# Optimization experiments

Hardware: AMD Instinct MI355X
Metric: run time of the kernel (lower is better)

The kernel has to match this reference:

```python
import jax, jax.numpy as jnp
import numpy as np

N, E, IN_DIM, H, C = 100000, 1600000, 128, 4, 64
NEG_SLOPE = 0.2
BN_EPS = 1e-5


def setup_inputs() -> dict:
    key = jax.random.key(0)
    ks = jax.random.split(key, 9)
    s = 1.0 / np.sqrt(IN_DIM)
    return {
        "feature": jax.random.normal(ks[0], (N, IN_DIM), dtype=jnp.float32),
        "edge_index": jax.random.randint(ks[1], (2, E), 0, N, dtype=jnp.int64),
        "W_l": jax.random.uniform(ks[2], (IN_DIM, H * C), jnp.float32, -s, s),
        "b_l": jnp.zeros((H * C,), jnp.float32),
        "W_r": jax.random.uniform(ks[3], (IN_DIM, H * C), jnp.float32, -s, s),
        "b_r": jnp.zeros((H * C,), jnp.float32),
        "att": jax.random.normal(ks[4], (H, C), dtype=jnp.float32) * 0.1,
        "bias": jnp.zeros((H * C,), jnp.float32),
        "gamma": jnp.ones((H * C,), jnp.float32),
        "beta": jnp.zeros((H * C,), jnp.float32),
    }


def reference(feature, edge_index, W_l, b_l, W_r, b_r, att, bias, gamma, beta):
    n = feature.shape[0]
    # add self loops (add_self_loops=True)
    loops = jnp.arange(n, dtype=edge_index.dtype)
    src = jnp.concatenate([edge_index[0], loops])
    dst = jnp.concatenate([edge_index[1], loops])
    # GATv2: separate source/target linear projections -> [N, H, C]
    x_l = (feature @ W_l + b_l).reshape(n, H, C)
    x_r = (feature @ W_r + b_r).reshape(n, H, C)
    # per-edge attention score: a^T LeakyReLU(x_l[src] + x_r[dst])  [Etot, H]
    e = jax.nn.leaky_relu(x_l[src] + x_r[dst], NEG_SLOPE)
    alpha = jnp.einsum('ehc,hc->eh', e, att)
    # segment softmax over incoming edges per target node
    amax = jax.ops.segment_max(alpha, dst, num_segments=n)  # [N, H]
    alpha = jnp.exp(alpha - amax[dst])
    denom = jax.ops.segment_sum(alpha, dst, num_segments=n)  # [N, H]
    alpha = alpha / (denom[dst] + 1e-16)
    # weighted scatter-aggregate of source messages
    out = jax.ops.segment_sum(x_l[src] * alpha[:, :, None], dst, num_segments=n)
    out = out.reshape(n, H * C) + bias  # concat=True
    # BatchNorm1d (training: batch statistics over nodes)
    mean = out.mean(axis=0)
    var = out.var(axis=0)
    out = (out - mean) / jnp.sqrt(var + BN_EPS) * gamma + beta
    return jax.nn.relu(out)
```

## Files before the change

### kernel.cpp

```cpp
#include <hip/hip_runtime.h>
#include <cstdint>

#define IN_DIM 128
#define HC 256
#define NEG_SLOPE 0.2f
#define BN_EPS 1e-5f
#define LOG2E 1.44269504088896340736f

#define B_HIST 1536
#define B_CW 32
#define B_FILL 512
#define CNT_STRIDE 16

typedef short bf16x8 __attribute__((ext_vector_type(8)));
typedef float f32x4 __attribute__((ext_vector_type(4)));

#define EXP2F(x) __builtin_amdgcn_exp2f(x)

__device__ __forceinline__ unsigned short f2bf(float f) {
    union { float f; unsigned int u; } v; v.f = f;
    unsigned int r = (v.u + 0x7FFFu + ((v.u >> 16) & 1u)) >> 16;
    return (unsigned short)r;
}
__device__ __forceinline__ float bf2f(unsigned short h) {
    union { unsigned int u; float f; } v; v.u = ((unsigned int)h) << 16;
    return v.f;
}

template<int CTRL>
__device__ __forceinline__ float dppadd(float x) {
    int y = __builtin_amdgcn_update_dpp(0, __builtin_bit_cast(int, x), CTRL, 0xF, 0xF, true);
    return x + __builtin_bit_cast(float, y);
}
__device__ __forceinline__ float red16(float p) {
    p = dppadd<0xB1>(p);
    p = dppadd<0x4E>(p);
    p = dppadd<0x124>(p);
    p = dppadd<0x128>(p);
    return p;
}

__device__ __forceinline__ void unpk(ushort4 u, float* f) {
    f[0] = bf2f(u.x); f[1] = bf2f(u.y); f[2] = bf2f(u.z); f[3] = bf2f(u.w);
}
__device__ __forceinline__ float esc(const float* f, float x0, float x1, float x2, float x3,
                                     float4 a) {
    float z0 = f[0] + x0, z1 = f[1] + x1, z2 = f[2] + x2, z3 = f[3] + x3;
    float p = a.x * fmaxf(z0, NEG_SLOPE * z0);
    p = fmaf(a.y, fmaxf(z1, NEG_SLOPE * z1), p);
    p = fmaf(a.z, fmaxf(z2, NEG_SLOPE * z2), p);
    p = fmaf(a.w, fmaxf(z3, NEG_SLOPE * z3), p);
    return p;
}

__global__ __launch_bounds__(256) void phase1(
    const float* __restrict__ F, unsigned short* __restrict__ Afrag,
    const float* __restrict__ Wl, const float* __restrict__ Wr,
    unsigned short* __restrict__ Wfrag,
    const int* __restrict__ ei, int* __restrict__ cnt, int* __restrict__ rank,
    int E, int n, int ntiles)
{
    int b = blockIdx.x;
    if (b < B_HIST) {
        for (int e = b * 256 + threadIdx.x; e < E; e += B_HIST * 256) {
            int dst = ei[(size_t)E + e];
            rank[e] = atomicAdd(&cnt[dst * CNT_STRIDE], 1);
        }
    } else if (b < B_HIST + B_CW) {
        int ob = (b - B_HIST) * 4 + (threadIdx.x >> 6);
        int j = ob >> 2;
        int kk = ob & 3;
        int l = threadIdx.x & 63;
        int col = j * 16 + (l & 15);
        const float* W = (col < 256) ? Wl : Wr;
        int c = col & 255;
        unsigned short tmp[8];
#pragma unroll
        for (int m = 0; m < 8; ++m) {
            int k = kk * 32 + ((l >> 4) << 3) + m;
            tmp[m] = f2bf(W[(size_t)k * 256 + c]);
        }
        ulonglong2* dst = (ulonglong2*)(Wfrag + ((size_t)(j * 4 + kk) * 64 + l) * 8);
        *dst = *(ulonglong2*)tmp;
    } else {
        int i = b - B_HIST - B_CW;
        int kk = threadIdx.x >> 6;
        int l = threadIdx.x & 63;
        int row = i * 16 + (l & 15);
        int k0 = kk * 32 + ((l >> 4) << 3);
        float4 f0 = make_float4(0.f, 0.f, 0.f, 0.f), f1 = f0;
        if (row < n) {
            const float* p = F + (size_t)row * IN_DIM + k0;
            f0 = *(const float4*)p;
            f1 = *(const float4*)(p + 4);
        }
        unsigned short tmp[8];
        tmp[0] = f2bf(f0.x); tmp[1] = f2bf(f0.y); tmp[2] = f2bf(f0.z); tmp[3] = f2bf(f0.w);
        tmp[4] = f2bf(f1.x); tmp[5] = f2bf(f1.y); tmp[6] = f2bf(f1.z); tmp[7] = f2bf(f1.w);
        ulonglong2* dst = (ulonglong2*)(Afrag + ((size_t)(i * 4 + kk) * 64 + l) * 8);
        *dst = *(ulonglong2*)tmp;
    }
}

#define SCAN_BLOCKS 256

__global__ __launch_bounds__(256) void scan_phaseA(const int* __restrict__ cnt,
                                                   int* __restrict__ blocksums,
                                                   int n, int ept)
{
    __shared__ int red[256];
    int t = threadIdx.x;
    int g = blockIdx.x * 256 + t;
    int beg = g * ept, end = min(beg + ept, n);
    int s = 0;
    for (int i = beg; i < end; ++i) s += cnt[i * CNT_STRIDE];
    red[t] = s;
    __syncthreads();
    for (int d = 128; d > 0; d >>= 1) {
        if (t < d) red[t] += red[t + d];
        __syncthreads();
    }
    if (t == 0) blocksums[blockIdx.x] = red[0];
}

__global__ __launch_bounds__(256) void scan_phaseC(const int* __restrict__ cnt,
                                                   const int* __restrict__ blocksums,
                                                   int* __restrict__ off,
                                                   int n, int ept)
{
    __shared__ int bs[256];
    __shared__ int sums[256];
    int t = threadIdx.x;
    bs[t] = blocksums[t];
    int g = blockIdx.x * 256 + t;
    int beg = g * ept, end = min(beg + ept, n);
    int s = 0;
    for (int i = beg; i < end; ++i) s += cnt[i * CNT_STRIDE];
    sums[t] = s;
    __syncthreads();
    for (int d = 1; d < 256; d <<= 1) {
        int v1 = (t >= d) ? sums[t - d] : 0;
        int v2 = (t >= d) ? bs[t - d] : 0;
        __syncthreads();
        sums[t] += v1;
        bs[t] += v2;
        __syncthreads();
    }
    int blockoff = (blockIdx.x == 0) ? 0 : bs[blockIdx.x - 1];
    int run = blockoff + ((t == 0) ? 0 : sums[t - 1]);
    for (int i = beg; i < end; ++i) {
        int c = cnt[i * CNT_STRIDE];
        off[i] = run;
        run += c;
    }
    if (blockIdx.x == 0 && t == 0) off[n] = bs[255];
}

__global__ __launch_bounds__(256) void phase2(
    const unsigned short* __restrict__ Afrag, const unsigned short* __restrict__ Wfrag,
    const float* __restrict__ bl, const float* __restrict__ br,
    unsigned short* __restrict__ xl, unsigned short* __restrict__ xr,
    const int* __restrict__ ei, const int* __restrict__ rank,
    const int* __restrict__ off, int* __restrict__ csr_boff,
    int E, int n, int ntiles)
{
    int b = blockIdx.x;
    if (b < B_FILL) {
        for (int e = b * 256 + threadIdx.x; e < E; e += B_FILL * 256) {
            int src = ei[e];
            int dst = ei[(size_t)E + e];
            int pos = off[dst] + rank[e];
            csr_boff[pos] = src << 9;
        }
    } else {
        int i = (b - B_FILL) * 4 + (threadIdx.x >> 6);
        if (i >= ntiles) return;
        int l = threadIdx.x & 63;

        const bf16x8* av = (const bf16x8*)(Afrag + ((size_t)i * 4 * 64 + l) * 8);
        bf16x8 a0 = av[0 * 64], a1 = av[1 * 64], a2 = av[2 * 64], a3 = av[3 * 64];

        const bf16x8* wv = (const bf16x8*)Wfrag + l;
        int cl = l & 15;
        int rbase = i * 16 + ((l >> 4) << 2);

#pragma unroll 4
        for (int j = 0; j < 32; ++j) {
            const bf16x8* bp = wv + (size_t)j * 4 * 64;
            f32x4 acc = {0.f, 0.f, 0.f, 0.f};
            acc = __builtin_amdgcn_mfma_f32_16x16x32_bf16(a0, bp[0 * 64], acc, 0, 0, 0);
            acc = __builtin_amdgcn_mfma_f32_16x16x32_bf16(a1, bp[1 * 64], acc, 0, 0, 0);
            acc = __builtin_amdgcn_mfma_f32_16x16x32_bf16(a2, bp[2 * 64], acc, 0, 0, 0);
            acc = __builtin_amdgcn_mfma_f32_16x16x32_bf16(a3, bp[3 * 64], acc, 0, 0, 0);

            int col = j * 16 + cl;
            unsigned short* X = (col < 256) ? xl : xr;
            int c = col & 255;
            float bv = (col < 256) ? bl[c] : br[c];
#pragma unroll
            for (int q = 0; q < 4; ++q) {
                int row = rbase + q;
                if (row < n) X[(size_t)row * HC + c] = f2bf(acc[q] + bv);
            }
        }
    }
}

__global__ __launch_bounds__(256) void gat_agg(
    const unsigned short* __restrict__ xl, const unsigned short* __restrict__ xr,
    const int* __restrict__ csr_boff, const int* __restrict__ off,
    const float* __restrict__ att, const float* __restrict__ bias,
    unsigned short* __restrict__ outb, int n)
{
    int d = (blockIdx.x * blockDim.x + threadIdx.x) >> 6;
    int lane = threadIdx.x & 63;
    if (d >= n) return;

    const char* xlc = (const char*)xl;
    int lo8 = lane << 3;
    ushort4 xru = ((const ushort4*)xr)[(size_t)d * 64 + lane];
    float xr0 = bf2f(xru.x), xr1 = bf2f(xru.y), xr2 = bf2f(xru.z), xr3 = bf2f(xru.w);
    float4 att4 = *(const float4*)(att + 4 * lane);
    att4.x *= LOG2E; att4.y *= LOG2E; att4.z *= LOG2E; att4.w *= LOG2E;

    int beg = __builtin_amdgcn_readfirstlane(off[d]);
    int end = __builtin_amdgcn_readfirstlane(off[d + 1]);

    float ax, ay, az, aw, lsum;
    {
        ushort4 t0 = *(const ushort4*)(xlc + ((size_t)d << 9) + lo8);
        float f0[4];
        unpk(t0, f0);
        float p0 = esc(f0, xr0, xr1, xr2, xr3, att4);
        p0 = red16(p0);
        float e0 = EXP2F(p0);
        ax = e0 * f0[0]; ay = e0 * f0[1]; az = e0 * f0[2]; aw = e0 * f0[3];
        lsum = e0;
    }

    int nmain = (end - beg) & ~3;
    int imend = beg + nmain;
    int i = beg;

    ushort4 u0, u1, u2, u3;
    if (i < imend) {
        int b0 = __builtin_amdgcn_readfirstlane(csr_boff[i]);
        int b1 = __builtin_amdgcn_readfirstlane(csr_boff[i + 1]);
        int b2 = __builtin_amdgcn_readfirstlane(csr_boff[i + 2]);
        int b3 = __builtin_amdgcn_readfirstlane(csr_boff[i + 3]);
        u0 = *(const ushort4*)(xlc + b0 + lo8);
        u1 = *(const ushort4*)(xlc + b1 + lo8);
        u2 = *(const ushort4*)(xlc + b2 + lo8);
        u3 = *(const ushort4*)(xlc + b3 + lo8);
    }
    while (i < imend) {
        ushort4 c0 = u0, c1 = u1, c2 = u2, c3 = u3;
        int inext = i + 4;
        if (inext < imend) {
            int b0 = __builtin_amdgcn_readfirstlane(csr_boff[inext]);
            int b1 = __builtin_amdgcn_readfirstlane(csr_boff[inext + 1]);
            int b2 = __builtin_amdgcn_readfirstlane(csr_boff[inext + 2]);
            int b3 = __builtin_amdgcn_readfirstlane(csr_boff[inext + 3]);
            u0 = *(const ushort4*)(xlc + b0 + lo8);
            u1 = *(const ushort4*)(xlc + b1 + lo8);
            u2 = *(const ushort4*)(xlc + b2 + lo8);
            u3 = *(const ushort4*)(xlc + b3 + lo8);
        }
        float f0[4], f1[4], f2[4], f3[4];
        unpk(c0, f0); unpk(c1, f1); unpk(c2, f2); unpk(c3, f3);

        float p0 = esc(f0, xr0, xr1, xr2, xr3, att4);
        float p1 = esc(f1, xr0, xr1, xr2, xr3, att4);
        float p2 = esc(f2, xr0, xr1, xr2, xr3, att4);
        float p3 = esc(f3, xr0, xr1, xr2, xr3, att4);

        p0 = dppadd<0xB1>(p0);  p1 = dppadd<0xB1>(p1);  p2 = dppadd<0xB1>(p2);  p3 = dppadd<0xB1>(p3);
        p0 = dppadd<0x4E>(p0);  p1 = dppadd<0x4E>(p1);  p2 = dppadd<0x4E>(p2);  p3 = dppadd<0x4E>(p3);
        p0 = dppadd<0x124>(p0); p1 = dppadd<0x124>(p1); p2 = dppadd<0x124>(p2); p3 = dppadd<0x124>(p3);
        p0 = dppadd<0x128>(p0); p1 = dppadd<0x128>(p1); p2 = dppadd<0x128>(p2); p3 = dppadd<0x128>(p3);

        float e0 = EXP2F(p0), e1 = EXP2F(p1);
        float e2 = EXP2F(p2), e3 = EXP2F(p3);
        ax = fmaf(e0, f0[0], fmaf(e1, f1[0], fmaf(e2, f2[0], fmaf(e3, f3[0], ax))));
        ay = fmaf(e0, f0[1], fmaf(e1, f1[1], fmaf(e2, f2[1], fmaf(e3, f3[1], ay))));
        az = fmaf(e0, f0[2], fmaf(e1, f1[2], fmaf(e2, f2[2], fmaf(e3, f3[2], az))));
        aw = fmaf(e0, f0[3], fmaf(e1, f1[3], fmaf(e2, f2[3], fmaf(e3, f3[3], aw))));
        lsum += (e0 + e1) + (e2 + e3);
        i = inext;
    }
    for (; i < end; ++i) {
        int b0 = __builtin_amdgcn_readfirstlane(csr_boff[i]);
        ushort4 t0 = *(const ushort4*)(xlc + b0 + lo8);
        float f0[4];
        unpk(t0, f0);
        float p0 = esc(f0, xr0, xr1, xr2, xr3, att4);
        p0 = red16(p0);
        float e0 = EXP2F(p0);
        ax = fmaf(e0, f0[0], ax); ay = fmaf(e0, f0[1], ay);
        az = fmaf(e0, f0[2], az); aw = fmaf(e0, f0[3], aw);
        lsum += e0;
    }

    float inv = 1.f / (lsum + 1e-16f);
    float4 b4 = *(const float4*)(bias + 4 * lane);
    ushort4 o;
    o.x = f2bf(fmaf(ax, inv, b4.x));
    o.y = f2bf(fmaf(ay, inv, b4.y));
    o.z = f2bf(fmaf(az, inv, b4.z));
    o.w = f2bf(fmaf(aw, inv, b4.w));
    ((ushort4*)outb)[(size_t)d * 64 + lane] = o;
}

#define NB_BN 1024
__global__ __launch_bounds__(256) void bn_partial(const unsigned short* __restrict__ outb,
                                                  float* __restrict__ partials, int n)
{
    int c = threadIdx.x;
    int b = blockIdx.x;
    int chunk = (n + NB_BN - 1) / NB_BN;
    int beg = b * chunk;
    int end = min(beg + chunk, n);
    float s = 0.f, s2 = 0.f;
    for (int r = beg; r < end; ++r) {
        float v = bf2f(outb[(size_t)r * HC + c]);
        s += v; s2 += v * v;
    }
    partials[(size_t)b * 512 + c] = s;
    partials[(size_t)b * 512 + 256 + c] = s2;
}

__global__ __launch_bounds__(256) void bn_final(const float* __restrict__ partials,
                                                float* __restrict__ stats, int n)
{
    int c = blockIdx.x;
    int t = threadIdx.x;
    float s = 0.f, s2 = 0.f;
    for (int b = t; b < NB_BN; b += 256) {
        s  += partials[(size_t)b * 512 + c];
        s2 += partials[(size_t)b * 512 + 256 + c];
    }
    __shared__ float rs[256], rs2[256];
    rs[t] = s; rs2[t] = s2;
    __syncthreads();
    for (int d = 128; d > 0; d >>= 1) {
        if (t < d) { rs[t] += rs[t + d]; rs2[t] += rs2[t + d]; }
        __syncthreads();
    }
    if (t == 0) {
        float mean = rs[0] / (float)n;
        float var = rs2[0] / (float)n - mean * mean;
        stats[c] = mean;
        stats[256 + c] = rsqrtf(var + BN_EPS);
    }
}

__global__ void bn_apply(const unsigned short* __restrict__ outb,
                         const float* __restrict__ stats,
                         const float* __restrict__ gamma, const float* __restrict__ beta,
                         float* __restrict__ out, long long total4)
{
    long long stride = (long long)gridDim.x * blockDim.x;
    for (long long i = blockIdx.x * (long long)blockDim.x + threadIdx.x; i < total4;
         i += stride) {
        int cb = ((int)(i & 63)) * 4;
        ushort4 u = ((const ushort4*)outb)[i];
        float4 o;
        o.x = fmaxf(0.f, (bf2f(u.x) - stats[cb + 0]) * stats[256 + cb + 0] * gamma[cb + 0] + beta[cb + 0]);
        o.y = fmaxf(0.f, (bf2f(u.y) - stats[cb + 1]) * stats[256 + cb + 1] * gamma[cb + 1] + beta[cb + 1]);
        o.z = fmaxf(0.f, (bf2f(u.z) - stats[cb + 2]) * stats[256 + cb + 2] * gamma[cb + 2] + beta[cb + 2]);
        o.w = fmaxf(0.f, (bf2f(u.w) - stats[cb + 3]) * stats[256 + cb + 3] * gamma[cb + 3] + beta[cb + 3]);
        ((float4*)out)[i] = o;
    }
}

extern "C" void kernel_launch(void* const* d_in, const int* in_sizes, int n_in,
                              void* d_out, int out_size, void* d_ws, size_t ws_size,
                              hipStream_t stream)
{
    const float* feature = (const float*)d_in[0];
    const int* ei        = (const int*)d_in[1];
    const float* Wl   = (const float*)d_in[2];
    const float* bl   = (const float*)d_in[3];
    const float* Wr   = (const float*)d_in[4];
    const float* br   = (const float*)d_in[5];
    const float* att  = (const float*)d_in[6];
    const float* bias = (const float*)d_in[7];
    const float* gamma = (const float*)d_in[8];
    const float* beta  = (const float*)d_in[9];

    const int n = in_sizes[0] / IN_DIM;
    const int E = in_sizes[1] / 2;
    const int ntiles = (n + 15) / 16;

    char* ws = (char*)d_ws;
    size_t o = 0;
    auto carve = [&](size_t bytes) -> void* {
        void* p = ws + o; o = (o + bytes + 15) & ~(size_t)15; return p;
    };
    unsigned short* xl    = (unsigned short*)carve((size_t)n * HC * sizeof(short));
    unsigned short* xr    = (unsigned short*)carve((size_t)n * HC * sizeof(short));
    unsigned short* outb  = (unsigned short*)carve((size_t)n * HC * sizeof(short));
    unsigned short* Afrag = (unsigned short*)carve((size_t)ntiles * 4 * 64 * 8 * sizeof(short));
    unsigned short* Wfrag = (unsigned short*)carve((size_t)32 * 4 * 64 * 8 * sizeof(short));
    int*   csr_boff = (int*)carve((size_t)E * sizeof(int));
    int*   rank    = (int*)carve((size_t)E * sizeof(int));
    int*   cnt     = (int*)carve((size_t)n * CNT_STRIDE * sizeof(int));
    int*   off     = (int*)carve((size_t)(n + 1) * sizeof(int));
    int*   blocksums = (int*)carve(SCAN_BLOCKS * sizeof(int));
    float* partials = (float*)carve((size_t)NB_BN * 512 * sizeof(float));
    float* stats   = (float*)carve(512 * sizeof(float));
    float* outf = (float*)d_out;

    if (o > ws_size) return;

    (void)hipMemsetAsync(cnt, 0, (size_t)n * CNT_STRIDE * sizeof(int), stream);

    phase1<<<B_HIST + B_CW + ntiles, 256, 0, stream>>>(
        feature, Afrag, Wl, Wr, Wfrag, ei, cnt, rank, E, n, ntiles);

    int ept = (n + SCAN_BLOCKS * 256 - 1) / (SCAN_BLOCKS * 256);
    scan_phaseA<<<SCAN_BLOCKS, 256, 0, stream>>>(cnt, blocksums, n, ept);
    scan_phaseC<<<SCAN_BLOCKS, 256, 0, stream>>>(cnt, blocksums, off, n, ept);

    phase2<<<B_FILL + (ntiles + 3) / 4, 256, 0, stream>>>(
        Afrag, Wfrag, bl, br, xl, xr, ei, rank, off, csr_boff, E, n, ntiles);

    int agg_blocks = (n + 3) / 4;
    gat_agg<<<agg_blocks, 256, 0, stream>>>(xl, xr, csr_boff, off, att, bias, outb, n);

    bn_partial<<<NB_BN, 256, 0, stream>>>(outb, partials, n);
    bn_final<<<256, 256, 0, stream>>>(partials, stats, n);
    long long total4 = (long long)n * (HC / 4);
    bn_apply<<<4096, 256, 0, stream>>>(outb, stats, gamma, beta, outf, total4);
}
```

Measured before the change: 368.6 us.

## Fuse GEMM into histogram kernel, fold BN partial sums into aggregation

Removes the Afrag staging buffer by converting features to bf16 fragments in registers and running the MFMA projection in the same launch as the degree histogram. The CSR fill becomes its own kernel, and the memset is replaced by a prep kernel that zeroes the counters and partials while building the weight fragments. BatchNorm sum and sum-of-squares are accumulated inside the aggregation kernel with shared-memory reduction and atomics into 64 striped buffers, which drops the separate pass that re-read outb. It also removes the 16-int padding on the histogram counters, so atomics on nearby destinations may now contend more.

```diff
diff --git a/kernel.cpp b/kernel.cpp
--- a/kernel.cpp
+++ b/kernel.cpp
@@ -8,9 +8,8 @@
 #define LOG2E 1.44269504088896340736f
 
 #define B_HIST 1536
-#define B_CW 32
-#define B_FILL 512
-#define CNT_STRIDE 16
+#define B_FILL 1024
+#define NBUF 64
 
 typedef short bf16x8 __attribute__((ext_vector_type(8)));
 typedef float f32x4 __attribute__((ext_vector_type(4)));
@@ -53,21 +52,14 @@
     return p;
 }
 
-__global__ __launch_bounds__(256) void phase1(
-    const float* __restrict__ F, unsigned short* __restrict__ Afrag,
+__global__ __launch_bounds__(256) void prep(
     const float* __restrict__ Wl, const float* __restrict__ Wr,
     unsigned short* __restrict__ Wfrag,
-    const int* __restrict__ ei, int* __restrict__ cnt, int* __restrict__ rank,
-    int E, int n, int ntiles)
+    int* __restrict__ cnt, float* __restrict__ partials, int n)
 {
     int b = blockIdx.x;
-    if (b < B_HIST) {
-        for (int e = b * 256 + threadIdx.x; e < E; e += B_HIST * 256) {
-            int dst = ei[(size_t)E + e];
-            rank[e] = atomicAdd(&cnt[dst * CNT_STRIDE], 1);
-        }
-    } else if (b < B_HIST + B_CW) {
-        int ob = (b - B_HIST) * 4 + (threadIdx.x >> 6);
+    if (b < 32) {
+        int ob = b * 4 + (threadIdx.x >> 6);
         int j = ob >> 2;
         int kk = ob & 3;
         int l = threadIdx.x & 63;
@@ -83,10 +75,36 @@
         ulonglong2* dst = (ulonglong2*)(Wfrag + ((size_t)(j * 4 + kk) * 64 + l) * 8);
         *dst = *(ulonglong2*)tmp;
     } else {
-        int i = b - B_HIST - B_CW;
-        int kk = threadIdx.x >> 6;
-        int l = threadIdx.x & 63;
-        int row = i * 16 + (l & 15);
+        int idx = (b - 32) * 256 + threadIdx.x;
+        int stride = 96 * 256;
+        for (int i = idx; i < n; i += stride) cnt[i] = 0;
+        for (int i = idx; i < NBUF * 1024; i += stride) partials[i] = 0.f;
+    }
+}
+
+__global__ __launch_bounds__(256) void phase_hg(
+    const float* __restrict__ F, const unsigned short* __restrict__ Wfrag,
+    const float* __restrict__ bl, const float* __restrict__ br,
+    unsigned short* __restrict__ xl, unsigned short* __restrict__ xr,
+    const int* __restrict__ ei, int* __restrict__ cnt, int* __restrict__ rank,
+    int E, int n, int ntiles)
+{
+    int b = blockIdx.x;
+    if (b < B_HIST) {
+        for (int e = b * 256 + threadIdx.x; e < E; e += B_HIST * 256) {
+            int dst = ei[(size_t)E + e];
+            rank[e] = atomicAdd(&cnt[dst], 1);
+        }
+        return;
+    }
+    int i = (b - B_HIST) * 4 + (threadIdx.x >> 6);
+    if (i >= ntiles) return;
+    int l = threadIdx.x & 63;
+
+    int row = i * 16 + (l & 15);
+    bf16x8 afr[4];
+#pragma unroll
+    for (int kk = 0; kk < 4; ++kk) {
         int k0 = kk * 32 + ((l >> 4) << 3);
         float4 f0 = make_float4(0.f, 0.f, 0.f, 0.f), f1 = f0;
         if (row < n) {
@@ -97,8 +115,31 @@
         unsigned short tmp[8];
         tmp[0] = f2bf(f0.x); tmp[1] = f2bf(f0.y); tmp[2] = f2bf(f0.z); tmp[3] = f2bf(f0.w);
         tmp[4] = f2bf(f1.x); tmp[5] = f2bf(f1.y); tmp[6] = f2bf(f1.z); tmp[7] = f2bf(f1.w);
-        ulonglong2* dst = (ulonglong2*)(Afrag + ((size_t)(i * 4 + kk) * 64 + l) * 8);
-        *dst = *(ulonglong2*)tmp;
+        afr[kk] = *(bf16x8*)tmp;
+    }
+
+    const bf16x8* wv = (const bf16x8*)Wfrag + l;
+    int cl = l & 15;
+    int rbase = i * 16 + ((l >> 4) << 2);
+
+#pragma unroll 4
+    for (int j = 0; j < 32; ++j) {
+        const bf16x8* bp = wv + (size_t)j * 4 * 64;
+        f32x4 acc = {0.f, 0.f, 0.f, 0.f};
+        acc = __builtin_amdgcn_mfma_f32_16x16x32_bf16(afr[0], bp[0 * 64], acc, 0, 0, 0);
+        acc = __builtin_amdgcn_mfma_f32_16x16x32_bf16(afr[1], bp[1 * 64], acc, 0, 0, 0);
+        acc = __builtin_amdgcn_mfma_f32_16x16x32_bf16(afr[2], bp[2 * 64], acc, 0, 0, 0);
+        acc = __builtin_amdgcn_mfma_f32_16x16x32_bf16(afr[3], bp[3 * 64], acc, 0, 0, 0);
+
+        int col = j * 16 + cl;
+        unsigned short* X = (col < 256) ? xl : xr;
+        int c = col & 255;
+        float bv = (col < 256) ? bl[c] : br[c];
+#pragma unroll
+        for (int q = 0; q < 4; ++q) {
+            int r = rbase + q;
+            if (r < n) X[(size_t)r * HC + c] = f2bf(acc[q] + bv);
+        }
     }
 }
 
@@ -113,7 +154,7 @@
     int g = blockIdx.x * 256 + t;
     int beg = g * ept, end = min(beg + ept, n);
     int s = 0;
-    for (int i = beg; i < end; ++i) s += cnt[i * CNT_STRIDE];
+    for (int i = beg; i < end; ++i) s += cnt[i];
     red[t] = s;
     __syncthreads();
     for (int d = 128; d > 0; d >>= 1) {
@@ -135,7 +176,7 @@
     int g = blockIdx.x * 256 + t;
     int beg = g * ept, end = min(beg + ept, n);
     int s = 0;
-    for (int i = beg; i < end; ++i) s += cnt[i * CNT_STRIDE];
+    for (int i = beg; i < end; ++i) s += cnt[i];
     sums[t] = s;
     __syncthreads();
     for (int d = 1; d < 256; d <<= 1) {
@@ -149,60 +190,23 @@
     int blockoff = (blockIdx.x == 0) ? 0 : bs[blockIdx.x - 1];
     int run = blockoff + ((t == 0) ? 0 : sums[t - 1]);
     for (int i = beg; i < end; ++i) {
-        int c = cnt[i * CNT_STRIDE];
+        int c = cnt[i];
         off[i] = run;
         run += c;
     }
     if (blockIdx.x == 0 && t == 0) off[n] = bs[255];
 }
 
-__global__ __launch_bounds__(256) void phase2(
-    const unsigned short* __restrict__ Afrag, const unsigned short* __restrict__ Wfrag,
-    const float* __restrict__ bl, const float* __restrict__ br,
-    unsigned short* __restrict__ xl, unsigned short* __restrict__ xr,
-    const int* __restrict__ ei, const int* __restrict__ rank,
-    const int* __restrict__ off, int* __restrict__ csr_boff,
-    int E, int n, int ntiles)
-{
-    int b = blockIdx.x;
-    if (b < B_FILL) {
-        for (int e = b * 256 + threadIdx.x; e < E; e += B_FILL * 256) {
-            int src = ei[e];
-            int dst = ei[(size_t)E + e];
-            int pos = off[dst] + rank[e];
-            csr_boff[pos] = src << 9;
-        }
-    } else {
-        int i = (b - B_FILL) * 4 + (threadIdx.x >> 6);
-        if (i >= ntiles) return;
-        int l = threadIdx.x & 63;
-
-        const bf16x8* av = (const bf16x8*)(Afrag + ((size_t)i * 4 * 64 + l) * 8);
-        bf16x8 a0 = av[0 * 64], a1 = av[1 * 64], a2 = av[2 * 64], a3 = av[3 * 64];
-
-        const bf16x8* wv = (const bf16x8*)Wfrag + l;
-        int cl = l & 15;
-        int rbase = i * 16 + ((l >> 4) << 2);
-
-#pragma unroll 4
-        for (int j = 0; j < 32; ++j) {
-            const bf16x8* bp = wv + (size_t)j * 4 * 64;
-            f32x4 acc = {0.f, 0.f, 0.f, 0.f};
-            acc = __builtin_amdgcn_mfma_f32_16x16x32_bf16(a0, bp[0 * 64], acc, 0, 0, 0);
-            acc = __builtin_amdgcn_mfma_f32_16x16x32_bf16(a1, bp[1 * 64], acc, 0, 0, 0);
-            acc = __builtin_amdgcn_mfma_f32_16x16x32_bf16(a2, bp[2 * 64], acc, 0, 0, 0);
-            acc = __builtin_amdgcn_mfma_f32_16x16x32_bf16(a3, bp[3 * 64], acc, 0, 0, 0);
-
-            int col = j * 16 + cl;
-            unsigned short* X = (col < 256) ? xl : xr;
-            int c = col & 255;
-            float bv = (col < 256) ? bl[c] : br[c];
-#pragma unroll
-            for (int q = 0; q < 4; ++q) {
-                int row = rbase + q;
-                if (row < n) X[(size_t)row * HC + c] = f2bf(acc[q] + bv);
-            }
-        }
+__global__ void fill_kernel(const int* __restrict__ ei, const int* __restrict__ rank,
+                            const int* __restrict__ off, int* __restrict__ csr_boff,
+                            int E)
+{
+    for (int e = blockIdx.x * blockDim.x + threadIdx.x; e < E;
+         e += gridDim.x * blockDim.x) {
+        int src = ei[e];
+        int dst = ei[(size_t)E + e];
+        int pos = off[dst] + rank[e];
+        csr_boff[pos] = src << 9;
     }
 }
 
@@ -210,148 +214,141 @@
     const unsigned short* __restrict__ xl, const unsigned short* __restrict__ xr,
     const int* __restrict__ csr_boff, const int* __restrict__ off,
     const float* __restrict__ att, const float* __restrict__ bias,
-    unsigned short* __restrict__ outb, int n)
-{
-    int d = (blockIdx.x * blockDim.x + threadIdx.x) >> 6;
+    unsigned short* __restrict__ outb, float* __restrict__ partials, int n)
+{
+    int w = threadIdx.x >> 6;
+    int d = blockIdx.x * 4 + w;
     int lane = threadIdx.x & 63;
-    if (d >= n) return;
-
-    const char* xlc = (const char*)xl;
-    int lo8 = lane << 3;
-    ushort4 xru = ((const ushort4*)xr)[(size_t)d * 64 + lane];
-    float xr0 = bf2f(xru.x), xr1 = bf2f(xru.y), xr2 = bf2f(xru.z), xr3 = bf2f(xru.w);
-    float4 att4 = *(const float4*)(att + 4 * lane);
-    att4.x *= LOG2E; att4.y *= LOG2E; att4.z *= LOG2E; att4.w *= LOG2E;
-
-    int beg = __builtin_amdgcn_readfirstlane(off[d]);
-    int end = __builtin_amdgcn_readfirstlane(off[d + 1]);
-
-    float ax, ay, az, aw, lsum;
-    {
-        ushort4 t0 = *(const ushort4*)(xlc + ((size_t)d << 9) + lo8);
-        float f0[4];
-        unpk(t0, f0);
-        float p0 = esc(f0, xr0, xr1, xr2, xr3, att4);
-        p0 = red16(p0);
-        float e0 = EXP2F(p0);
-        ax = e0 * f0[0]; ay = e0 * f0[1]; az = e0 * f0[2]; aw = e0 * f0[3];
-        lsum = e0;
-    }
-
-    int nmain = (end - beg) & ~3;
-    int imend = beg + nmain;
-    int i = beg;
-
-    ushort4 u0, u1, u2, u3;
-    if (i < imend) {
-        int b0 = __builtin_amdgcn_readfirstlane(csr_boff[i]);
-        int b1 = __builtin_amdgcn_readfirstlane(csr_boff[i + 1]);
-        int b2 = __builtin_amdgcn_readfirstlane(csr_boff[i + 2]);
-        int b3 = __builtin_amdgcn_readfirstlane(csr_boff[i + 3]);
-        u0 = *(const ushort4*)(xlc + b0 + lo8);
-        u1 = *(const ushort4*)(xlc + b1 + lo8);
-        u2 = *(const ushort4*)(xlc + b2 + lo8);
-        u3 = *(const ushort4*)(xlc + b3 + lo8);
-    }
-    while (i < imend) {
-        ushort4 c0 = u0, c1 = u1, c2 = u2, c3 = u3;
-        int inext = i + 4;
-        if (inext < imend) {
-            int b0 = __builtin_amdgcn_readfirstlane(csr_boff[inext]);
-            int b1 = __builtin_amdgcn_readfirstlane(csr_boff[inext + 1]);
-            int b2 = __builtin_amdgcn_readfirstlane(csr_boff[inext + 2]);
-            int b3 = __builtin_amdgcn_readfirstlane(csr_boff[inext + 3]);
+    bool active = (d < n);
+
+    float vx = 0.f, vy = 0.f, vz = 0.f, vw = 0.f;
+
+    if (active) {
+        const char* xlc = (const char*)xl;
+        int lo8 = lane << 3;
+        ushort4 xru = ((const ushort4*)xr)[(size_t)d * 64 + lane];
+        float xr0 = bf2f(xru.x), xr1 = bf2f(xru.y), xr2 = bf2f(xru.z), xr3 = bf2f(xru.w);
+        float4 att4 = *(const float4*)(att + 4 * lane);
+        att4.x *= LOG2E; att4.y *= LOG2E; att4.z *= LOG2E; att4.w *= LOG2E;
+
+        int beg = __builtin_amdgcn_readfirstlane(off[d]);
+        int end = __builtin_amdgcn_readfirstlane(off[d + 1]);
+
+        float ax, ay, az, aw, lsum;
+        {
+            ushort4 t0 = *(const ushort4*)(xlc + ((size_t)d << 9) + lo8);
+            float f0[4];
+            unpk(t0, f0);
+            float p0 = esc(f0, xr0, xr1, xr2, xr3, att4);
+            p0 = red16(p0);
+            float e0 = EXP2F(p0);
+            ax = e0 * f0[0]; ay = e0 * f0[1]; az = e0 * f0[2]; aw = e0 * f0[3];
+            lsum = e0;
+        }
+
+        int nmain = (end - beg) & ~3;
+        int imend = beg + nmain;
+        int i = beg;
+
+        ushort4 u0, u1, u2, u3;
+        if (i < imend) {
+            int b0 = __builtin_amdgcn_readfirstlane(csr_boff[i]);
+            int b1 = __builtin_amdgcn_readfirstlane(csr_boff[i + 1]);
+            int b2 = __builtin_amdgcn_readfirstlane(csr_boff[i + 2]);
+            int b3 = __builtin_amdgcn_readfirstlane(csr_boff[i + 3]);
             u0 = *(const ushort4*)(xlc + b0 + lo8);
             u1 = *(const ushort4*)(xlc + b1 + lo8);
             u2 = *(const ushort4*)(xlc + b2 + lo8);
             u3 = *(const ushort4*)(xlc + b3 + lo8);
         }
-        float f0[4], f1[4], f2[4], f3[4];
-        unpk(c0, f0); unpk(c1, f1); unpk(c2, f2); unpk(c3, f3);
-
-        float p0 = esc(f0, xr0, xr1, xr2, xr3, att4);
-        float p1 = esc(f1, xr0, xr1, xr2, xr3, att4);
-        float p2 = esc(f2, xr0, xr1, xr2, xr3, att4);
-        float p3 = esc(f3, xr0, xr1, xr2, xr3, att4);
-
-        p0 = dppadd<0xB1>(p0);  p1 = dppadd<0xB1>(p1);  p2 = dppadd<0xB1>(p2);  p3 = dppadd<0xB1>(p3);
-        p0 = dppadd<0x4E>(p0);  p1 = dppadd<0x4E>(p1);  p2 = dppadd<0x4E>(p2);  p3 = dppadd<0x4E>(p3);
-        p0 = dppadd<0x124>(p0); p1 = dppadd<0x124>(p1); p2 = dppadd<0x124>(p2); p3 = dppadd<0x124>(p3);
-        p0 = dppadd<0x128>(p0); p1 = dppadd<0x128>(p1); p2 = dppadd<0x128>(p2); p3 = dppadd<0x128>(p3);
-
-        float e0 = EXP2F(p0), e1 = EXP2F(p1);
-        float e2 = EXP2F(p2), e3 = EXP2F(p3);
-        ax = fmaf(e0, f0[0], fmaf(e1, f1[0], fmaf(e2, f2[0], fmaf(e3, f3[0], ax))));
-        ay = fmaf(e0, f0[1], fmaf(e1, f1[1], fmaf(e2, f2[1], fmaf(e3, f3[1], ay))));
-        az = fmaf(e0, f0[2], fmaf(e1, f1[2], fmaf(e2, f2[2], fmaf(e3, f3[2], az))));
-        aw = fmaf(e0, f0[3], fmaf(e1, f1[3], fmaf(e2, f2[3], fmaf(e3, f3[3], aw))));
-        lsum += (e0 + e1) + (e2 + e3);
-        i = inext;
-    }
-    for (; i < end; ++i) {
-        int b0 = __builtin_amdgcn_readfirstlane(csr_boff[i]);
-        ushort4 t0 = *(const ushort4*)(xlc + b0 + lo8);
-        float f0[4];
-        unpk(t0, f0);
-        float p0 = esc(f0, xr0, xr1, xr2, xr3, att4);
-        p0 = red16(p0);
-        float e0 = EXP2F(p0);
-        ax = fmaf(e0, f0[0], ax); ay = fmaf(e0, f0[1], ay);
-        az = fmaf(e0, f0[2], az); aw = fmaf(e0, f0[3], aw);
-        lsum += e0;
-    }
-
-    float inv = 1.f / (lsum + 1e-16f);
-    float4 b4 = *(const float4*)(bias + 4 * lane);
-    ushort4 o;
-    o.x = f2bf(fmaf(ax, inv, b4.x));
-    o.y = f2bf(fmaf(ay, inv, b4.y));
-    o.z = f2bf(fmaf(az, inv, b4.z));
-    o.w = f2bf(fmaf(aw, inv, b4.w));
-    ((ushort4*)outb)[(size_t)d * 64 + lane] = o;
-}
-
-#define NB_BN 1024
-__global__ __launch_bounds__(256) void bn_partial(const unsigned short* __restrict__ outb,
-                                                  float* __restrict__ partials, int n)
-{
-    int c = threadIdx.x;
-    int b = blockIdx.x;
-    int chunk = (n + NB_BN - 1) / NB_BN;
-    int beg = b * chunk;
-    int end = min(beg + chunk, n);
-    float s = 0.f, s2 = 0.f;
-    for (int r = beg; r < end; ++r) {
-        float v = bf2f(outb[(size_t)r * HC + c]);
-        s += v; s2 += v * v;
-    }
-    partials[(size_t)b * 512 + c] = s;
-    partials[(size_t)b * 512 + 256 + c] = s2;
+        while (i < imend) {
+            ushort4 c0 = u0, c1 = u1, c2 = u2, c3 = u3;
+            int inext = i + 4;
+            if (inext < imend) {
+                int b0 = __builtin_amdgcn_readfirstlane(csr_boff[inext]);
+                int b1 = __builtin_amdgcn_readfirstlane(csr_boff[inext + 1]);
+                int b2 = __builtin_amdgcn_readfirstlane(csr_boff[inext + 2]);
+                int b3 = __builtin_amdgcn_readfirstlane(csr_boff[inext + 3]);
+                u0 = *(const ushort4*)(xlc + b0 + lo8);
+                u1 = *(const ushort4*)(xlc + b1 + lo8);
+                u2 = *(const ushort4*)(xlc + b2 + lo8);
+                u3 = *(const ushort4*)(xlc + b3 + lo8);
+            }
+            float f0[4], f1[4], f2[4], f3[4];
+            unpk(c0, f0); unpk(c1, f1); unpk(c2, f2); unpk(c3, f3);
+
+            float p0 = esc(f0, xr0, xr1, xr2, xr3, att4);
+            float p1 = esc(f1, xr0, xr1, xr2, xr3, att4);
+            float p2 = esc(f2, xr0, xr1, xr2, xr3, att4);
+            float p3 = esc(f3, xr0, xr1, xr2, xr3, att4);
+
+            p0 = dppadd<0xB1>(p0);  p1 = dppadd<0xB1>(p1);  p2 = dppadd<0xB1>(p2);  p3 = dppadd<0xB1>(p3);
+            p0 = dppadd<0x4E>(p0);  p1 = dppadd<0x4E>(p1);  p2 = dppadd<0x4E>(p2);  p3 = dppadd<0x4E>(p3);
+            p0 = dppadd<0x124>(p0); p1 = dppadd<0x124>(p1); p2 = dppadd<0x124>(p2); p3 = dppadd<0x124>(p3);
+            p0 = dppadd<0x128>(p0); p1 = dppadd<0x128>(p1); p2 = dppadd<0x128>(p2); p3 = dppadd<0x128>(p3);
+
+            float e0 = EXP2F(p0), e1 = EXP2F(p1);
+            float e2 = EXP2F(p2), e3 = EXP2F(p3);
+            ax = fmaf(e0, f0[0], fmaf(e1, f1[0], fmaf(e2, f2[0], fmaf(e3, f3[0], ax))));
+            ay = fmaf(e0, f0[1], fmaf(e1, f1[1], fmaf(e2, f2[1], fmaf(e3, f3[1], ay))));
+            az = fmaf(e0, f0[2], fmaf(e1, f1[2], fmaf(e2, f2[2], fmaf(e3, f3[2], az))));
+            aw = fmaf(e0, f0[3], fmaf(e1, f1[3], fmaf(e2, f2[3], fmaf(e3, f3[3], aw))));
+            lsum += (e0 + e1) + (e2 + e3);
+            i = inext;
+        }
+        for (; i < end; ++i) {
+            int b0 = __builtin_amdgcn_readfirstlane(csr_boff[i]);
+            ushort4 t0 = *(const ushort4*)(xlc + b0 + lo8);
+            float f0[4];
+            unpk(t0, f0);
+            float p0 = esc(f0, xr0, xr1, xr2, xr3, att4);
+            p0 = red16(p0);
+            float e0 = EXP2F(p0);
+            ax = fmaf(e0, f0[0], ax); ay = fmaf(e0, f0[1], ay);
+            az = fmaf(e0, f0[2], az); aw = fmaf(e0, f0[3], aw);
+            lsum += e0;
+        }
+
+        float inv = 1.f / (lsum + 1e-16f);
+        float4 b4 = *(const float4*)(bias + 4 * lane);
+        vx = fmaf(ax, inv, b4.x);
+        vy = fmaf(ay, inv, b4.y);
+        vz = fmaf(az, inv, b4.z);
+        vw = fmaf(aw, inv, b4.w);
+        ushort4 o;
+        o.x = f2bf(vx); o.y = f2bf(vy); o.z = f2bf(vz); o.w = f2bf(vw);
+        ((ushort4*)outb)[(size_t)d * 64 + lane] = o;
+        vx = bf2f(o.x); vy = bf2f(o.y); vz = bf2f(o.z); vw = bf2f(o.w);
+    }
+
+    __shared__ float sv[4 * 512];
+    int c0 = (lane << 2);
+    float* svw = sv + w * 512;
+    svw[c0 + 0] = vx; svw[c0 + 1] = vy; svw[c0 + 2] = vz; svw[c0 + 3] = vw;
+    svw[256 + c0 + 0] = vx * vx; svw[256 + c0 + 1] = vy * vy;
+    svw[256 + c0 + 2] = vz * vz; svw[256 + c0 + 3] = vw * vw;
+    __syncthreads();
+    int t = threadIdx.x;
+    float S = sv[t] + sv[512 + t] + sv[1024 + t] + sv[1536 + t];
+    float Q = sv[256 + t] + sv[768 + t] + sv[1280 + t] + sv[1792 + t];
+    float* pb = partials + (size_t)(blockIdx.x & (NBUF - 1)) * 1024;
+    atomicAdd(&pb[t], S);
+    atomicAdd(&pb[512 + t], Q);
 }
 
 __global__ __launch_bounds__(256) void bn_final(const float* __restrict__ partials,
                                                 float* __restrict__ stats, int n)
 {
-    int c = blockIdx.x;
-    int t = threadIdx.x;
+    int c = threadIdx.x;
     float s = 0.f, s2 = 0.f;
-    for (int b = t; b < NB_BN; b += 256) {
-        s  += partials[(size_t)b * 512 + c];
-        s2 += partials[(size_t)b * 512 + 256 + c];
-    }
-    __shared__ float rs[256], rs2[256];
-    rs[t] = s; rs2[t] = s2;
-    __syncthreads();
-    for (int d = 128; d > 0; d >>= 1) {
-        if (t < d) { rs[t] += rs[t + d]; rs2[t] += rs2[t + d]; }
-        __syncthreads();
-    }
-    if (t == 0) {
-        float mean = rs[0] / (float)n;
-        float var = rs2[0] / (float)n - mean * mean;
-        stats[c] = mean;
-        stats[256 + c] = rsqrtf(var + BN_EPS);
-    }
+    for (int b = 0; b < NBUF; ++b) {
+        s  += partials[(size_t)b * 1024 + c];
+        s2 += partials[(size_t)b * 1024 + 512 + c];
+    }
+    float mean = s / (float)n;
+    float var = s2 / (float)n - mean * mean;
+    stats[c] = mean;
+    stats[256 + c] = rsqrtf(var + BN_EPS);
 }
 
 __global__ void bn_apply(const unsigned short* __restrict__ outb,
@@ -400,36 +397,34 @@
     unsigned short* xl    = (unsigned short*)carve((size_t)n * HC * sizeof(short));
     unsigned short* xr    = (unsigned short*)carve((size_t)n * HC * sizeof(short));
     unsigned short* outb  = (unsigned short*)carve((size_t)n * HC * sizeof(short));
-    unsigned short* Afrag = (unsigned short*)carve((size_t)ntiles * 4 * 64 * 8 * sizeof(short));
     unsigned short* Wfrag = (unsigned short*)carve((size_t)32 * 4 * 64 * 8 * sizeof(short));
     int*   csr_boff = (int*)carve((size_t)E * sizeof(int));
     int*   rank    = (int*)carve((size_t)E * sizeof(int));
-    int*   cnt     = (int*)carve((size_t)n * CNT_STRIDE * sizeof(int));
+    int*   cnt     = (int*)carve((size_t)n * sizeof(int));
     int*   off     = (int*)carve((size_t)(n + 1) * sizeof(int));
     int*   blocksums = (int*)carve(SCAN_BLOCKS * sizeof(int));
-    float* partials = (float*)carve((size_t)NB_BN * 512 * sizeof(float));
+    float* partials = (float*)carve((size_t)NBUF * 1024 * sizeof(float));
     float* stats   = (float*)carve(512 * sizeof(float));
     float* outf = (float*)d_out;
 
     if (o > ws_size) return;
 
-    (void)hipMemsetAsync(cnt, 0, (size_t)n * CNT_STRIDE * sizeof(int), stream);
-
-    phase1<<<B_HIST + B_CW + ntiles, 256, 0, stream>>>(
-        feature, Afrag, Wl, Wr, Wfrag, ei, cnt, rank, E, n, ntiles);
+    prep<<<128, 256, 0, stream>>>(Wl, Wr, Wfrag, cnt, partials, n);
+
+    phase_hg<<<B_HIST + (ntiles + 3) / 4, 256, 0, stream>>>(
+        feature, Wfrag, bl, br, xl, xr, ei, cnt, rank, E, n, ntiles);
 
     int ept = (n + SCAN_BLOCKS * 256 - 1) / (SCAN_BLOCKS * 256);
     scan_phaseA<<<SCAN_BLOCKS, 256, 0, stream>>>(cnt, blocksums, n, ept);
     scan_phaseC<<<SCAN_BLOCKS, 256, 0, stream>>>(cnt, blocksums, off, n, ept);
 
-    phase2<<<B_FILL + (ntiles + 3) / 4, 256, 0, stream>>>(
-        Afrag, Wfrag, bl, br, xl, xr, ei, rank, off, csr_boff, E, n, ntiles);
+    fill_kernel<<<B_FILL, 256, 0, stream>>>(ei, rank, off, csr_boff, E);
 
     int agg_blocks = (n + 3) / 4;
-    gat_agg<<<agg_blocks, 256, 0, stream>>>(xl, xr, csr_boff, off, att, bias, outb, n);
-
-    bn_partial<<<NB_BN, 256, 0, stream>>>(outb, partials, n);
-    bn_final<<<256, 256, 0, stream>>>(partials, stats, n);
+    gat_agg<<<agg_blocks, 256, 0, stream>>>(xl, xr, csr_boff, off, att, bias,
+                                            outb, partials, n);
+
+    bn_final<<<1, 256, 0, stream>>>(partials, stats, n);
     long long total4 = (long long)n * (HC / 4);
     bn_apply<<<4096, 256, 0, stream>>>(outb, stats, gamma, beta, outf, total4);
 }
```

Result: faster. 345.5 us (-6.3%).
